# Optimization experiments

Hardware: AMD Instinct MI355X
Metric: run time of the kernel (lower is better)

Reference implementation:

```python
import jax, jax.numpy as jnp
import numpy as np

N = 4096; E = 32768; S = 64; V = 16; H0 = 64; H1 = 16; STEPS = 3
SQRT3 = float(np.sqrt(3.0))


def _tp(sx, vx, sy, vy):
    # full CG tensor product restricted to paths landing in 0e/1o
    # sx [n,m0], vx [n,m1,3], sy [n,k0], vy [n,k1,3]
    n = sx.shape[0]
    ss = (sx[:, :, None] * sy[:, None, :]).reshape(n, -1)              # 0e x 0e -> 0e
    dd = (jnp.einsum('nmi,nki->nmk', vx, vy) / SQRT3).reshape(n, -1)    # 1o . 1o -> 0e
    sv = (sx[:, :, None, None] * vy[:, None, :, :]).reshape(n, -1, 3)   # 0e x 1o -> 1o
    vs = (vx[:, :, None, :] * sy[:, None, :, None]).reshape(n, -1, 3)   # 1o x 0e -> 1o
    return jnp.concatenate([ss, dd], -1), jnp.concatenate([sv, vs], -2)


def _tpl_gate(sx, vx, sy, vy, ws, b, wv, n0):
    # TensorProductLinearGate: tensor_product -> Linear -> gate
    s_tp, v_tp = _tp(sx, vx, sy, vy)
    s = s_tp @ ws + b                                  # scalars + gate scalars
    v = jnp.einsum('ntd,tm->nmd', v_tp, wv)
    scal = jax.nn.gelu(s[:, :n0])
    gates = jax.nn.sigmoid(s[:, n0:])
    return scal, v * gates[:, :, None]


def _seg_mean(x, idx, n):
    s = jax.ops.segment_sum(x, idx, num_segments=n)
    c = jax.ops.segment_sum(jnp.ones((x.shape[0],), x.dtype), idx, num_segments=n)
    c = jnp.maximum(c, 1.0).reshape((n,) + (1,) * (x.ndim - 1))
    return s / c


def setup_inputs() -> dict:
    key = jax.random.key(0)
    ks = jax.random.split(key, 20)
    f32 = jnp.float32

    def w(k, shape):
        return jax.random.normal(k, shape, f32) / np.sqrt(shape[-2]).astype(np.float32)

    def bias(k, shape):
        return 0.1 * jax.random.normal(k, shape, f32)

    E1 = 2 * (S + V)          # 160: edge block0 TP width
    E2 = H0 + H1              # 80: edge blocks 1-2 TP width
    K0 = H0 + 1; K1 = H1 + 1  # message concat sh
    N0TP = S * K0 + V * K1    # 4432
    N1TP = S * K1 + V * K0    # 2128
    return {
        'node_s': jax.random.normal(ks[0], (N, S), f32),
        'node_v': jax.random.normal(ks[1], (N, V, 3), f32),
        'senders': jax.random.randint(ks[2], (E,), 0, N, jnp.int32),
        'receivers': jax.random.randint(ks[3], (E,), 0, N, jnp.int32),
        'e1_ws': w(ks[4], (STEPS, E1, H0 + H1)),
        'e1_b': bias(ks[5], (STEPS, H0 + H1)),
        'e1_wv': w(ks[6], (STEPS, E1, H1)),
        'e2_ws': w(ks[7], (STEPS, 2, E2, H0 + H1)),
        'e2_b': bias(ks[8], (STEPS, 2, H0 + H1)),
        'e2_wv': w(ks[9], (STEPS, 2, E2, H1)),
        'n_ws': w(ks[10], (STEPS, 3, N0TP, S + V)),
        'n_b': bias(ks[11], (STEPS, 3, S + V)),
        'n_wv': w(ks[12], (STEPS, 3, N1TP, V)),
        'l_ws': w(ks[13], (STEPS, S, S)),
        'l_b': bias(ks[14], (STEPS, S)),
        'l_wv': w(ks[15], (STEPS, V, V)),
    }


def reference(node_s, node_v, senders, receivers, e1_ws, e1_b, e1_wv,
              e2_ws, e2_b, e2_wv, n_ws, n_b, n_wv, l_ws, l_b, l_wv):
    norm = float(E - 1)
    for step in range(STEPS):
        s_i, v_i = node_s[senders], node_v[senders]
        s_j, v_j = node_s[receivers], node_v[receivers]
        r = v_i[:, 0] - v_j[:, 0]                    # slice_by_mul[:1] = positions
        rn = jnp.linalg.norm(r, axis=-1, keepdims=True)
        unit = r / jnp.maximum(rn, 1e-9)
        a_s = jnp.ones((E, 1), node_s.dtype)          # Y_0, component norm
        a_v = (SQRT3 * unit)[:, None, :]              # Y_1, component norm
        m_s = jnp.concatenate([s_i, s_j], -1)
        m_v = jnp.concatenate([v_i, v_j], -2)
        for blk in range(3):
            if blk == 0:
                ws, b, wv = e1_ws[step], e1_b[step], e1_wv[step]
            else:
                ws, b, wv = e2_ws[step, blk - 1], e2_b[step, blk - 1], e2_wv[step, blk - 1]
            m_s, m_v = _tpl_gate(m_s, m_v, a_s, a_v, ws, b, wv, H0)
        # ---- aggregate (segment_mean) + normalize_messages ----
        ms = _seg_mean(m_s, receivers, N) / norm
        mv = _seg_mean(m_v, receivers, N) / norm
        as_ = _seg_mean(a_s, receivers, N) / norm
        av = _seg_mean(a_v, receivers, N) / norm
        y_s = jnp.concatenate([ms, as_], -1)          # [N, H0+1]
        y_v = jnp.concatenate([mv, av], -2)           # [N, H1+1, 3]
        for blk in range(3):
            node_s, node_v = _tpl_gate(node_s, node_v, y_s, y_v,
                                       n_ws[step, blk], n_b[step, blk], n_wv[step, blk], S)
        # ---- final per-step Linear(irreps_in) ----
        node_s = node_s @ l_ws[step] + l_b[step]
        node_v = jnp.einsum('nmd,mk->nkd', node_v, l_wv[step])
    return jnp.concatenate([node_v.reshape(node_v.shape[0], -1), node_s], -1)
```

## Files before the change

### kernel.cpp

```cpp
#include <hip/hip_runtime.h>
#include <math.h>

constexpr int NND = 4096;
constexpr int EDG = 32768;
constexpr float SQRT3  = 1.7320508075688772f;
constexpr float ISQRT3 = 0.5773502691896258f;
constexpr float NORMI  = 1.0f / 32767.0f;

__device__ __forceinline__ float gelu_f(float x) {
    float x3 = x * x * x;
    return 0.5f * x * (1.0f + tanhf(0.7978845608028654f * (x + 0.044715f * x3)));
}
__device__ __forceinline__ float sigmoid_f(float x) {
    return 1.0f / (1.0f + expf(-x));
}

__global__ __launch_bounds__(256)
void segnn_deg_kernel(const int* __restrict__ rcv, int* __restrict__ deg) {
    const int e = blockIdx.x * 256 + threadIdx.x;
    if (e < EDG) atomicAdd(deg + rcv[e], 1);
}

__global__ __launch_bounds__(1024)
void segnn_scan_kernel(const int* __restrict__ deg, int* __restrict__ off) {
    __shared__ int tots[1024];
    const int t = threadIdx.x;
    const int v0 = deg[4*t], v1 = deg[4*t+1], v2 = deg[4*t+2], v3 = deg[4*t+3];
    const int p1 = v0, p2 = p1 + v1, p3 = p2 + v2, p4 = p3 + v3;
    tots[t] = p4;
    __syncthreads();
    for (int d = 1; d < 1024; d <<= 1) {
        const int add = (t >= d) ? tots[t - d] : 0;
        __syncthreads();
        tots[t] += add;
        __syncthreads();
    }
    const int excl = t ? tots[t-1] : 0;
    off[4*t+0] = excl;
    off[4*t+1] = excl + p1;
    off[4*t+2] = excl + p2;
    off[4*t+3] = excl + p3;
    if (t == 1023) off[4096] = tots[1023];
}

__global__ __launch_bounds__(256)
void segnn_scatter_kernel(const int* __restrict__ rcv, const int* __restrict__ off,
                          int* __restrict__ cursor, int* __restrict__ elist) {
    const int e = blockIdx.x * 256 + threadIdx.x;
    if (e < EDG) {
        const int j = rcv[e];
        const int p = atomicAdd(cursor + j, 1);
        elist[off[j] + p] = e;
    }
}

template<int NSX, int NVX>
__device__ __forceinline__ void edge_phase_w(
    const int lane,
    const float* __restrict__ Ws, const float* __restrict__ Bs,
    const float* __restrict__ Wv,
    float (*xt)[10], float (*x2)[10], float (*cb)[96], float (*cvv)[48])
{
    const int cs = lane & 15, kg = lane >> 4;
    constexpr int KA = NSX + NVX;
    constexpr int CH = KA / 4;

    {
        float acc[8][6];
#pragma unroll
        for (int j = 0; j < 8; ++j)
#pragma unroll
            for (int c = 0; c < 6; ++c) acc[j][c] = 0.0f;
        const int r0 = kg * CH;
#pragma unroll 4
        for (int rr = 0; rr < CH; ++rr) {
            const int r = r0 + rr;
            const float* wp = Ws + r*80 + cs;
            const float w0 = wp[0], w1 = wp[16], w2 = wp[32], w3 = wp[48], w4 = wp[64];
            const float w5 = (r < NSX) ? Wv[r*16 + cs] : 0.0f;
            const float2 xa = *reinterpret_cast<const float2*>(&xt[r][0]);
            const float2 xb = *reinterpret_cast<const float2*>(&xt[r][2]);
            const float2 xc = *reinterpret_cast<const float2*>(&xt[r][4]);
            const float2 xd = *reinterpret_cast<const float2*>(&xt[r][6]);
            const float xe[8] = { xa.x,xa.y, xb.x,xb.y, xc.x,xc.y, xd.x,xd.y };
#pragma unroll
            for (int j = 0; j < 8; ++j) {
                acc[j][0] = fmaf(xe[j], w0, acc[j][0]);
                acc[j][1] = fmaf(xe[j], w1, acc[j][1]);
                acc[j][2] = fmaf(xe[j], w2, acc[j][2]);
                acc[j][3] = fmaf(xe[j], w3, acc[j][3]);
                acc[j][4] = fmaf(xe[j], w4, acc[j][4]);
                acc[j][5] = fmaf(xe[j], w5, acc[j][5]);
            }
        }
#pragma unroll
        for (int j = 0; j < 8; ++j)
#pragma unroll
            for (int c = 0; c < 6; ++c) {
                float a = acc[j][c];
                a += __shfl_xor(a, 16);
                a += __shfl_xor(a, 32);
                acc[j][c] = a;
            }
        if (lane < 16) {
#pragma unroll
            for (int j = 0; j < 8; ++j) {
#pragma unroll
                for (int c = 0; c < 5; ++c) cb[j][cs + 16*c] = acc[j][c] + Bs[cs + 16*c];
                cb[j][80 + cs] = acc[j][5];
            }
        }
    }

    {
        constexpr int CHB = NVX / 4;
        float av[8][3];
#pragma unroll
        for (int j = 0; j < 8; ++j) { av[j][0]=0.0f; av[j][1]=0.0f; av[j][2]=0.0f; }
        const int m0 = kg * CHB;
#pragma unroll
        for (int mm = 0; mm < CHB; ++mm) {
            const int m = m0 + mm;
            const float w = Wv[(NSX + m)*16 + cs];
#pragma unroll
            for (int d = 0; d < 3; ++d) {
                const float2 xa = *reinterpret_cast<const float2*>(&x2[d*NVX + m][0]);
                const float2 xb = *reinterpret_cast<const float2*>(&x2[d*NVX + m][2]);
                const float2 xc = *reinterpret_cast<const float2*>(&x2[d*NVX + m][4]);
                const float2 xd = *reinterpret_cast<const float2*>(&x2[d*NVX + m][6]);
                const float xe[8] = { xa.x,xa.y, xb.x,xb.y, xc.x,xc.y, xd.x,xd.y };
#pragma unroll
                for (int j = 0; j < 8; ++j) av[j][d] = fmaf(xe[j], w, av[j][d]);
            }
        }
#pragma unroll
        for (int j = 0; j < 8; ++j)
#pragma unroll
            for (int d = 0; d < 3; ++d) {
                float a = av[j][d];
                a += __shfl_xor(a, 16);
                a += __shfl_xor(a, 32);
                av[j][d] = a;
            }
        if (lane < 16) {
#pragma unroll
            for (int j = 0; j < 8; ++j)
#pragma unroll
                for (int d = 0; d < 3; ++d) cvv[j][cs*3 + d] = av[j][d];
        }
    }
    asm volatile("" ::: "memory");
}

__global__ __launch_bounds__(256, 2)
void segnn_edge_fused(const float* __restrict__ cs, const float* __restrict__ cv,
                      const int* __restrict__ snd, const int* __restrict__ rcv,
                      const float* __restrict__ W0s, const float* __restrict__ B0, const float* __restrict__ W0v,
                      const float* __restrict__ W1s, const float* __restrict__ B1, const float* __restrict__ W1v,
                      const float* __restrict__ W2s, const float* __restrict__ B2, const float* __restrict__ W2v,
                      float* __restrict__ msg) {
    __shared__ __align__(16) float XT [4][160][10];
    __shared__ __align__(16) float X2T[4][96][10];
    __shared__ __align__(16) float Cb [4][8][96];
    __shared__ __align__(16) float Cv [4][8][48];
    __shared__ float UU [4][8][4];

    const int tid  = threadIdx.x;
    const int w    = tid >> 6;
    const int lane = tid & 63;
    const int e0   = blockIdx.x * 32 + w * 8;

    float (*xt)[10]  = XT[w];
    float (*x2)[10]  = X2T[w];
    float (*cb)[96]  = Cb[w];
    float (*cvv)[48] = Cv[w];
    float (*uuw)[4]  = UU[w];

#pragma unroll
    for (int it = 0; it < 16; ++it) {
        const int e = it >> 1, half = it & 1;
        const int node = (half ? rcv : snd)[e0 + e];
        xt[half*64 + lane][e] = cs[(size_t)node*64 + lane];
    }
#pragma unroll
    for (int it = 0; it < 16; ++it) {
        const int e = it >> 1, half = it & 1;
        if (lane < 48) {
            const int node = (half ? rcv : snd)[e0 + e];
            const int m = lane / 3, d = lane - 3*m;
            x2[d*32 + half*16 + m][e] = cv[(size_t)node*48 + lane];
        }
    }
    asm volatile("" ::: "memory");
    if (lane < 8) {
        const float rx = x2[0][lane]  - x2[16][lane];
        const float ry = x2[32][lane] - x2[48][lane];
        const float rz = x2[64][lane] - x2[80][lane];
        const float rinv = 1.0f / fmaxf(sqrtf(rx*rx+ry*ry+rz*rz), 1e-9f);
        uuw[lane][0] = rx*rinv; uuw[lane][1] = ry*rinv; uuw[lane][2] = rz*rinv;
    }
    asm volatile("" ::: "memory");
#pragma unroll
    for (int it = 0; it < 4; ++it) {
        const int idx = it*64 + lane;
        const int e = idx >> 5, mm = idx & 31;
        xt[128 + mm][e] = x2[mm][e]*uuw[e][0] + x2[32+mm][e]*uuw[e][1] + x2[64+mm][e]*uuw[e][2];
    }
    asm volatile("" ::: "memory");

    edge_phase_w<128,32>(lane, W0s, B0, W0v, xt, x2, cb, cvv);
#pragma unroll
    for (int it = 0; it < 8; ++it) {
        xt[lane][it] = gelu_f(cb[it][lane]);
    }
#pragma unroll
    for (int it = 0; it < 2; ++it) {
        const int idx = it*64 + lane;
        const int e = idx >> 4, o = idx & 15;
        const float g = sigmoid_f(cb[e][64+o]);
        const float t = cb[e][80+o] * SQRT3;
        float p = 0.0f;
#pragma unroll
        for (int d = 0; d < 3; ++d) {
            const float vd = fmaf(t, uuw[e][d], cvv[e][o*3+d]) * g;
            x2[d*16 + o][e] = vd;
            p = fmaf(vd, uuw[e][d], p);
        }
        xt[64 + o][e] = p;
    }
    asm volatile("" ::: "memory");

    edge_phase_w<64,16>(lane, W1s, B1, W1v, xt, x2, cb, cvv);
#pragma unroll
    for (int it = 0; it < 8; ++it) {
        xt[lane][it] = gelu_f(cb[it][lane]);
    }
#pragma unroll
    for (int it = 0; it < 2; ++it) {
        const int idx = it*64 + lane;
        const int e = idx >> 4, o = idx & 15;
        const float g = sigmoid_f(cb[e][64+o]);
        const float t = cb[e][80+o] * SQRT3;
        float p = 0.0f;
#pragma unroll
        for (int d = 0; d < 3; ++d) {
            const float vd = fmaf(t, uuw[e][d], cvv[e][o*3+d]) * g;
            x2[d*16 + o][e] = vd;
            p = fmaf(vd, uuw[e][d], p);
        }
        xt[64 + o][e] = p;
    }
    asm volatile("" ::: "memory");

    edge_phase_w<64,16>(lane, W2s, B2, W2v, xt, x2, cb, cvv);
#pragma unroll
    for (int it = 0; it < 15; ++it) {
        const int idx = it*64 + lane;
        if (idx < 920) {
            const int e = idx / 115, f = idx - 115*e;
            float vv;
            if (f < 64) {
                vv = gelu_f(cb[e][f]);
            } else if (f < 112) {
                const int q = f - 64, o = q / 3, d = q - 3*o;
                const float g = sigmoid_f(cb[e][64+o]);
                vv = fmaf(cb[e][80+o] * SQRT3, uuw[e][d], cvv[e][q]) * g;
            } else {
                vv = uuw[e][f-112];
            }
            msg[(size_t)(e0+e)*116 + f] = vv;
        }
    }
}

__global__ __launch_bounds__(128)
void segnn_gather_kernel(const float* __restrict__ msg, const int* __restrict__ off,
                         const int* __restrict__ elist,
                         float* __restrict__ y_s, float* __restrict__ y_v) {
    const int n = blockIdx.x, f = threadIdx.x;
    const int o0 = off[n], o1 = off[n+1];
    const int deg = o1 - o0;
    float acc = 0.0f;
    for (int p = o0; p < o1; ++p) {
        const int eid = elist[p];
        if (f < 115) acc += msg[(size_t)eid*116 + f];
    }
    const float inv = NORMI / (float)(deg > 0 ? deg : 1);
    if (f < 64)        y_s[(size_t)n*65 + f] = acc * inv;
    else if (f < 112)  y_v[(size_t)n*51 + (f-64)] = acc * inv;
    else if (f < 115)  y_v[(size_t)n*51 + 48 + (f-112)] = SQRT3 * acc * inv;
    else if (f == 115) y_s[(size_t)n*65 + 64] = deg ? NORMI : 0.0f;
}

__global__ __launch_bounds__(512, 2)
void segnn_node_kernel(const float* __restrict__ in_s, const float* __restrict__ in_v,
                       const float* __restrict__ y_s, const float* __restrict__ y_v,
                       const float* __restrict__ W,  const float* __restrict__ B,
                       const float* __restrict__ Wv,
                       float* __restrict__ out_s, float* __restrict__ out_v) {
    __shared__ __align__(16) float xsL[8*65];
    __shared__ __align__(16) float ysL[8*65];
    __shared__ __align__(16) float xvL[8*49];
    __shared__ __align__(16) float yvL[8*51];
    __shared__ __align__(16) float Xa[2][3072];
    __shared__ __align__(16) float red[8][16][41];
    __shared__ float finGG[8*16];

    const int tid  = threadIdx.x;
    const int lane = tid & 63;
    const int wv   = tid >> 6;
    const int nb0  = blockIdx.x * 8;

    for (int idx = tid; idx < 8*64; idx += 512) { const int n = idx >> 6, m = idx & 63; xsL[n*65+m] = in_s[(size_t)(nb0+n)*64 + m]; }
    for (int idx = tid; idx < 8*65; idx += 512) { const int n = idx / 65, k = idx - n*65; ysL[n*65+k] = y_s[(size_t)(nb0+n)*65 + k]; }
    for (int idx = tid; idx < 8*48; idx += 512) { const int n = idx / 48, m = idx - n*48; xvL[n*49+m] = in_v[(size_t)(nb0+n)*48 + m]; }
    for (int idx = tid; idx < 8*51; idx += 512) { const int n = idx / 51, m = idx - n*51; yvL[n*51+m] = y_v[(size_t)(nb0+n)*51 + m]; }
    __syncthreads();

    {
        const int cs = tid & 15;
        const int rowgrp = tid >> 4;

        float acc[8][5];
#pragma unroll
        for (int n = 0; n < 8; ++n)
#pragma unroll
            for (int c = 0; c < 5; ++c) acc[n][c] = 0.0f;

        auto genS = [&](int t, int b) {
            const int base = t * 128;
#pragma unroll
            for (int ii = 0; ii < 2; ++ii) {
                const int idx = tid + ii*512;
                const int rl = idx >> 3, n = idx & 7;
                const int r = base + rl;
                float val = 0.0f;
                if (r < 4160) {
                    const int m = r / 65, k = r - m*65;
                    val = xsL[n*65+m] * ysL[n*65+k];
                } else if (r < 4432) {
                    const int q = r - 4160;
                    const int m = q / 17, k = q - m*17;
                    val = (xvL[n*49+m*3+0]*yvL[n*51+k*3+0] +
                           xvL[n*49+m*3+1]*yvL[n*51+k*3+1] +
                           xvL[n*49+m*3+2]*yvL[n*51+k*3+2]) * ISQRT3;
                }
                Xa[b][idx] = val;
            }
        };
        auto loadW = [&](int t, float wreg[4][5]) {
            const int base = t * 128;
#pragma unroll
            for (int v2 = 0; v2 < 4; ++v2) {
                const int r = base + rowgrp + 32*v2;
                const int wr = r < 4431 ? r : 4431;
                const float* wp = W + (size_t)wr * 80 + cs;
                wreg[v2][0] = wp[0];  wreg[v2][1] = wp[16]; wreg[v2][2] = wp[32];
                wreg[v2][3] = wp[48]; wreg[v2][4] = wp[64];
            }
        };

        float wc[4][5], wn[4][5];
        loadW(0, wc);
        genS(0, 0);
        asm volatile("s_waitcnt lgkmcnt(0)" ::: "memory");
        __builtin_amdgcn_s_barrier();
        asm volatile("" ::: "memory");
        for (int t = 0; t < 35; ++t) {
            if (t + 1 < 35) { loadW(t + 1, wn); genS(t + 1, (t + 1) & 1); }
            const float* Xb = &Xa[t & 1][0];
#pragma unroll
            for (int v2 = 0; v2 < 4; ++v2) {
                const int rl = rowgrp + 32*v2;
                const float4 xq0 = *reinterpret_cast<const float4*>(&Xb[rl*8]);
                const float4 xq1 = *reinterpret_cast<const float4*>(&Xb[rl*8+4]);
                const float xn[8] = { xq0.x, xq0.y, xq0.z, xq0.w, xq1.x, xq1.y, xq1.z, xq1.w };
#pragma unroll
                for (int n = 0; n < 8; ++n) {
                    acc[n][0] = fmaf(xn[n], wc[v2][0], acc[n][0]);
                    acc[n][1] = fmaf(xn[n], wc[v2][1], acc[n][1]);
                    acc[n][2] = fmaf(xn[n], wc[v2][2], acc[n][2]);
                    acc[n][3] = fmaf(xn[n], wc[v2][3], acc[n][3]);
                    acc[n][4] = fmaf(xn[n], wc[v2][4], acc[n][4]);
                }
            }
            asm volatile("s_waitcnt lgkmcnt(0)" ::: "memory");
            __builtin_amdgcn_s_barrier();
            asm volatile("" ::: "memory");
#pragma unroll
            for (int v2 = 0; v2 < 4; ++v2)
#pragma unroll
                for (int c = 0; c < 5; ++c) wc[v2][c] = wn[v2][c];
        }

#pragma unroll
        for (int n = 0; n < 8; ++n)
#pragma unroll
            for (int c = 0; c < 5; ++c) {
                float a = acc[n][c];
                a += __shfl_xor(a, 16);
                a += __shfl_xor(a, 32);
                if (lane < 16) red[wv][lane][n*5+c] = a;
            }
        __syncthreads();
        for (int idx = tid; idx < 8*80; idx += 512) {
            const int n = idx / 80, col = idx - n*80;
            const int cs2 = col & 15, ci2 = col >> 4;
            float s = B[col];
#pragma unroll
            for (int ww = 0; ww < 8; ++ww) s += red[ww][cs2][n*5+ci2];
            if (col < 64) out_s[(size_t)(nb0+n)*64 + col] = gelu_f(s);
            else          finGG[n*16 + (col-64)] = s;
        }
        __syncthreads();
    }

    {
        const int j4 = tid & 3;
        const int ngrp = (tid >> 2) & 1;
        const int rg = tid >> 3;

        float av[12][4];
#pragma unroll
        for (int a = 0; a < 12; ++a)
#pragma unroll
            for (int c = 0; c < 4; ++c) av[a][c] = 0.0f;

        auto genV = [&](int t, int b) {
            const int base = t * 128;
#pragma unroll
            for (int ii = 0; ii < 6; ++ii) {
                const int idx = tid + ii*512;
                const int rl = idx / 24, ar = idx - rl*24;
                const int n = ar / 3, d = ar - n*3;
                const int r = base + rl;
                float val = 0.0f;
                if (r < 1088) {
                    const int m = r / 17, k = r - m*17;
                    val = xsL[n*65+m] * yvL[n*51+k*3+d];
                } else if (r < 2128) {
                    const int q = r - 1088;
                    const int m = q / 65, k = q - m*65;
                    val = xvL[n*49+m*3+d] * ysL[n*65+k];
                }
                Xa[b][idx] = val;
            }
        };
        auto loadWv = [&](int t, float4 wreg[2]) {
#pragma unroll
            for (int v2 = 0; v2 < 2; ++v2) {
                const int r = t*128 + rg + 64*v2;
                const int wr = r < 2127 ? r : 2127;
                wreg[v2] = *reinterpret_cast<const float4*>(&Wv[(size_t)wr*16 + 4*j4]);
            }
        };

        float4 wqc[2], wqn[2];
        loadWv(0, wqc);
        genV(0, 0);
        asm volatile("s_waitcnt lgkmcnt(0)" ::: "memory");
        __builtin_amdgcn_s_barrier();
        asm volatile("" ::: "memory");
        for (int t = 0; t < 17; ++t) {
            if (t + 1 < 17) { loadWv(t + 1, wqn); genV(t + 1, (t + 1) & 1); }
            const float* Xb = &Xa[t & 1][0];
#pragma unroll
            for (int v2 = 0; v2 < 2; ++v2) {
                const int rl = rg + 64*v2;
                const float4 w4 = wqc[v2];
                const float4 xq0 = *reinterpret_cast<const float4*>(&Xb[rl*24 + 12*ngrp]);
                const float4 xq1 = *reinterpret_cast<const float4*>(&Xb[rl*24 + 12*ngrp + 4]);
                const float4 xq2 = *reinterpret_cast<const float4*>(&Xb[rl*24 + 12*ngrp + 8]);
                const float xr[12] = { xq0.x,xq0.y,xq0.z,xq0.w, xq1.x,xq1.y,xq1.z,xq1.w, xq2.x,xq2.y,xq2.z,xq2.w };
#pragma unroll
                for (int a = 0; a < 12; ++a) {
                    av[a][0] = fmaf(xr[a], w4.x, av[a][0]);
                    av[a][1] = fmaf(xr[a], w4.y, av[a][1]);
                    av[a][2] = fmaf(xr[a], w4.z, av[a][2]);
                    av[a][3] = fmaf(xr[a], w4.w, av[a][3]);
                }
            }
            asm volatile("s_waitcnt lgkmcnt(0)" ::: "memory");
            __builtin_amdgcn_s_barrier();
            asm volatile("" ::: "memory");
            wqc[0] = wqn[0]; wqc[1] = wqn[1];
        }

        float* redf = &red[0][0][0];
#pragma unroll
        for (int a = 0; a < 12; ++a)
#pragma unroll
            for (int c = 0; c < 4; ++c) {
                float x = av[a][c];
                x += __shfl_xor(x, 8);
                x += __shfl_xor(x, 16);
                x += __shfl_xor(x, 32);
                if (lane < 8) redf[wv*392 + lane*49 + a*4 + c] = x;
            }
        __syncthreads();
        for (int idx = tid; idx < 24*16; idx += 512) {
            const int ar = idx >> 4, j = idx & 15;
            const int n = ar / 3, d = ar - n*3;
            const int ng2 = ar / 12, a2 = ar - 12*ng2;
            const int jj4 = j >> 2, c2 = j & 3;
            float s = 0.0f;
#pragma unroll
            for (int ww = 0; ww < 8; ++ww) s += redf[ww*392 + (jj4 + 4*ng2)*49 + a2*4 + c2];
            out_v[(size_t)(nb0+n)*48 + j*3 + d] = s * sigmoid_f(finGG[n*16 + j]);
        }
    }
}

__global__ __launch_bounds__(256)
void segnn_linear_kernel(const float* __restrict__ in_s, const float* __restrict__ in_v,
                         const float* __restrict__ lws, const float* __restrict__ lb,
                         const float* __restrict__ lwv,
                         float* __restrict__ out_s, float* __restrict__ out_v,
                         float* __restrict__ out_cat) {
    const int idx = blockIdx.x * 256 + threadIdx.x;
    if (idx >= NND * 112) return;
    const int nidx = idx / 112, f = idx - nidx * 112;
    if (f < 48) {
        const int k = f / 3, d = f - 3*k;
        const float* vp = in_v + (size_t)nidx * 48 + d;
        float acc = 0.0f;
#pragma unroll
        for (int m = 0; m < 16; ++m) acc = fmaf(vp[m*3], lwv[m*16 + k], acc);
        if (out_cat) out_cat[(size_t)nidx*112 + f] = acc;
        else         out_v[(size_t)nidx*48 + f] = acc;
    } else {
        const int o = f - 48;
        const float* sp = in_s + (size_t)nidx * 64;
        float acc = lb[o];
#pragma unroll
        for (int m = 0; m < 64; ++m) acc = fmaf(sp[m], lws[m*64 + o], acc);
        if (out_cat) out_cat[(size_t)nidx*112 + f] = acc;
        else         out_s[(size_t)nidx*64 + o] = acc;
    }
}

extern "C" void kernel_launch(void* const* d_in, const int* in_sizes, int n_in,
                              void* d_out, int out_size, void* d_ws, size_t ws_size,
                              hipStream_t stream) {
    const float* in_s  = (const float*)d_in[0];
    const float* in_v  = (const float*)d_in[1];
    const int*   snd   = (const int*)  d_in[2];
    const int*   rcv   = (const int*)  d_in[3];
    const float* e1_ws = (const float*)d_in[4];
    const float* e1_b  = (const float*)d_in[5];
    const float* e1_wv = (const float*)d_in[6];
    const float* e2_ws = (const float*)d_in[7];
    const float* e2_b  = (const float*)d_in[8];
    const float* e2_wv = (const float*)d_in[9];
    const float* n_ws  = (const float*)d_in[10];
    const float* n_b   = (const float*)d_in[11];
    const float* n_wv  = (const float*)d_in[12];
    const float* l_ws  = (const float*)d_in[13];
    const float* l_b   = (const float*)d_in[14];
    const float* l_wv  = (const float*)d_in[15];

    float* ws    = (float*)d_ws;
    float* cur_s = ws;
    float* cur_v = cur_s + 262144;
    float* nxt_s = cur_v + 196608;
    float* nxt_v = nxt_s + 262144;
    float* y_s   = nxt_v + 196608;
    float* y_v   = y_s + 266240;
    float* msg   = y_v + 208896;
    int*   deg    = (int*)(msg + 3801088);
    int*   cursor = deg + 4096;
    int*   off    = cursor + 4096;
    int*   elist  = off + 4097;

    hipMemsetAsync(deg, 0, (size_t)8192 * sizeof(int), stream);
    hipMemcpyAsync(cur_s, in_s, (size_t)262144 * sizeof(float), hipMemcpyDeviceToDevice, stream);
    hipMemcpyAsync(cur_v, in_v, (size_t)196608 * sizeof(float), hipMemcpyDeviceToDevice, stream);
    segnn_deg_kernel<<<EDG/256, 256, 0, stream>>>(rcv, deg);
    segnn_scan_kernel<<<1, 1024, 0, stream>>>(deg, off);
    segnn_scatter_kernel<<<EDG/256, 256, 0, stream>>>(rcv, off, cursor, elist);

    for (int step = 0; step < 3; ++step) {
        segnn_edge_fused<<<EDG/32, 256, 0, stream>>>(cur_s, cur_v, snd, rcv,
            e1_ws + (size_t)step*160*80, e1_b + step*80, e1_wv + (size_t)step*160*16,
            e2_ws + (size_t)(step*2+0)*80*80, e2_b + (step*2+0)*80, e2_wv + (size_t)(step*2+0)*80*16,
            e2_ws + (size_t)(step*2+1)*80*80, e2_b + (step*2+1)*80, e2_wv + (size_t)(step*2+1)*80*16,
            msg);
        segnn_gather_kernel<<<NND, 128, 0, stream>>>(msg, off, elist, y_s, y_v);

        segnn_node_kernel<<<NND/8, 512, 0, stream>>>(cur_s, cur_v, y_s, y_v,
            n_ws + (size_t)(step*3+0)*4432*80, n_b + (step*3+0)*80, n_wv + (size_t)(step*3+0)*2128*16,
            nxt_s, nxt_v);
        segnn_node_kernel<<<NND/8, 512, 0, stream>>>(nxt_s, nxt_v, y_s, y_v,
            n_ws + (size_t)(step*3+1)*4432*80, n_b + (step*3+1)*80, n_wv + (size_t)(step*3+1)*2128*16,
            cur_s, cur_v);
        segnn_node_kernel<<<NND/8, 512, 0, stream>>>(cur_s, cur_v, y_s, y_v,
            n_ws + (size_t)(step*3+2)*4432*80, n_b + (step*3+2)*80, n_wv + (size_t)(step*3+2)*2128*16,
            nxt_s, nxt_v);

        segnn_linear_kernel<<<(NND*112 + 255)/256, 256, 0, stream>>>(nxt_s, nxt_v,
            l_ws + (size_t)step*64*64, l_b + step*64, l_wv + (size_t)step*16*16,
            cur_s, cur_v, (step == 2) ? (float*)d_out : nullptr);
    }
}
```

Before: 1.301 ms.

## Drop weight register prefetch, raise node kernel occupancy, swizzle scalar LDS tile

Result: faster. 1.065 ms (-18.1%).

```diff
diff --git a/kernel.cpp b/kernel.cpp
--- a/kernel.cpp
+++ b/kernel.cpp
@@ -292,7 +292,7 @@
     else if (f == 115) y_s[(size_t)n*65 + 64] = deg ? NORMI : 0.0f;
 }
 
-__global__ __launch_bounds__(512, 2)
+__global__ __launch_bounds__(512, 4)
 void segnn_node_kernel(const float* __restrict__ in_s, const float* __restrict__ in_v,
                        const float* __restrict__ y_s, const float* __restrict__ y_v,
                        const float* __restrict__ W,  const float* __restrict__ B,
@@ -345,52 +345,37 @@
                            xvL[n*49+m*3+1]*yvL[n*51+k*3+1] +
                            xvL[n*49+m*3+2]*yvL[n*51+k*3+2]) * ISQRT3;
                 }
-                Xa[b][idx] = val;
+                Xa[b][idx ^ (((idx >> 8) & 3) << 3)] = val;
             }
         };
-        auto loadW = [&](int t, float wreg[4][5]) {
+
+        genS(0, 0);
+        __syncthreads();
+        for (int t = 0; t < 35; ++t) {
+            if (t + 1 < 35) genS(t + 1, (t + 1) & 1);
             const int base = t * 128;
+            const float* Xb = &Xa[t & 1][0];
 #pragma unroll
             for (int v2 = 0; v2 < 4; ++v2) {
-                const int r = base + rowgrp + 32*v2;
+                const int rl = rowgrp + 32*v2;
+                const int r  = base + rl;
                 const int wr = r < 4431 ? r : 4431;
                 const float* wp = W + (size_t)wr * 80 + cs;
-                wreg[v2][0] = wp[0];  wreg[v2][1] = wp[16]; wreg[v2][2] = wp[32];
-                wreg[v2][3] = wp[48]; wreg[v2][4] = wp[64];
-            }
-        };
-
-        float wc[4][5], wn[4][5];
-        loadW(0, wc);
-        genS(0, 0);
-        asm volatile("s_waitcnt lgkmcnt(0)" ::: "memory");
-        __builtin_amdgcn_s_barrier();
-        asm volatile("" ::: "memory");
-        for (int t = 0; t < 35; ++t) {
-            if (t + 1 < 35) { loadW(t + 1, wn); genS(t + 1, (t + 1) & 1); }
-            const float* Xb = &Xa[t & 1][0];
-#pragma unroll
-            for (int v2 = 0; v2 < 4; ++v2) {
-                const int rl = rowgrp + 32*v2;
-                const float4 xq0 = *reinterpret_cast<const float4*>(&Xb[rl*8]);
-                const float4 xq1 = *reinterpret_cast<const float4*>(&Xb[rl*8+4]);
+                const float w0 = wp[0], w1 = wp[16], w2 = wp[32], w3 = wp[48], w4_ = wp[64];
+                const int sb = (rl*8) ^ (((rl >> 5) & 3) << 3);
+                const float4 xq0 = *reinterpret_cast<const float4*>(&Xb[sb]);
+                const float4 xq1 = *reinterpret_cast<const float4*>(&Xb[sb+4]);
                 const float xn[8] = { xq0.x, xq0.y, xq0.z, xq0.w, xq1.x, xq1.y, xq1.z, xq1.w };
 #pragma unroll
                 for (int n = 0; n < 8; ++n) {
-                    acc[n][0] = fmaf(xn[n], wc[v2][0], acc[n][0]);
-                    acc[n][1] = fmaf(xn[n], wc[v2][1], acc[n][1]);
-                    acc[n][2] = fmaf(xn[n], wc[v2][2], acc[n][2]);
-                    acc[n][3] = fmaf(xn[n], wc[v2][3], acc[n][3]);
-                    acc[n][4] = fmaf(xn[n], wc[v2][4], acc[n][4]);
+                    acc[n][0] = fmaf(xn[n], w0,  acc[n][0]);
+                    acc[n][1] = fmaf(xn[n], w1,  acc[n][1]);
+                    acc[n][2] = fmaf(xn[n], w2,  acc[n][2]);
+                    acc[n][3] = fmaf(xn[n], w3,  acc[n][3]);
+                    acc[n][4] = fmaf(xn[n], w4_, acc[n][4]);
                 }
             }
-            asm volatile("s_waitcnt lgkmcnt(0)" ::: "memory");
-            __builtin_amdgcn_s_barrier();
-            asm volatile("" ::: "memory");
-#pragma unroll
-            for (int v2 = 0; v2 < 4; ++v2)
-#pragma unroll
-                for (int c = 0; c < 5; ++c) wc[v2][c] = wn[v2][c];
+            __syncthreads();
         }
 
 #pragma unroll
@@ -446,28 +431,18 @@
                 Xa[b][idx] = val;
             }
         };
-        auto loadWv = [&](int t, float4 wreg[2]) {
-#pragma unroll
-            for (int v2 = 0; v2 < 2; ++v2) {
-                const int r = t*128 + rg + 64*v2;
-                const int wr = r < 2127 ? r : 2127;
-                wreg[v2] = *reinterpret_cast<const float4*>(&Wv[(size_t)wr*16 + 4*j4]);
-            }
-        };
-
-        float4 wqc[2], wqn[2];
-        loadWv(0, wqc);
+
         genV(0, 0);
-        asm volatile("s_waitcnt lgkmcnt(0)" ::: "memory");
-        __builtin_amdgcn_s_barrier();
-        asm volatile("" ::: "memory");
+        __syncthreads();
         for (int t = 0; t < 17; ++t) {
-            if (t + 1 < 17) { loadWv(t + 1, wqn); genV(t + 1, (t + 1) & 1); }
+            if (t + 1 < 17) genV(t + 1, (t + 1) & 1);
             const float* Xb = &Xa[t & 1][0];
 #pragma unroll
             for (int v2 = 0; v2 < 2; ++v2) {
                 const int rl = rg + 64*v2;
-                const float4 w4 = wqc[v2];
+                const int r  = t*128 + rl;
+                const int wr = r < 2127 ? r : 2127;
+                const float4 w4 = *reinterpret_cast<const float4*>(&Wv[(size_t)wr*16 + 4*j4]);
                 const float4 xq0 = *reinterpret_cast<const float4*>(&Xb[rl*24 + 12*ngrp]);
                 const float4 xq1 = *reinterpret_cast<const float4*>(&Xb[rl*24 + 12*ngrp + 4]);
                 const float4 xq2 = *reinterpret_cast<const float4*>(&Xb[rl*24 + 12*ngrp + 8]);
@@ -480,10 +455,7 @@
                     av[a][3] = fmaf(xr[a], w4.w, av[a][3]);
                 }
             }
-            asm volatile("s_waitcnt lgkmcnt(0)" ::: "memory");
-            __builtin_amdgcn_s_barrier();
-            asm volatile("" ::: "memory");
-            wqc[0] = wqn[0]; wqc[1] = wqn[1];
+            __syncthreads();
         }
 
         float* redf = &red[0][0][0];
```
